# Performance work log

Measured on AMD Instinct MI355X. Metric: run time of the kernel, lower is better.

The kernel has to match this reference:

```python
import jax, jax.numpy as jnp
import numpy as np

# Module constants (from init_kwargs + mp_num=8 from the mesh)
D_MODEL = 1024
N_HEAD = 16
D_HEAD = 64
D_ROT = 64
MP = 8
B, S = 2, 2048
LOCAL = N_HEAD * D_HEAD // MP          # 128 : per-mp-shard qkv dim
F_IN = N_HEAD * D_HEAD * 3 + D_MODEL * 8  # 11264 : fused qkv+ff projection width
D_OUT_IN = D_MODEL + 4 * D_MODEL       # 5120 : attn (1024) + glu (4096) into output_proj
LN_EPS = 1e-5


def _rotate_every_two(x):
    # x: [..., d] with d even -> interleaved (-x2, x1)
    x1 = x[..., ::2]
    x2 = x[..., 1::2]
    return jnp.stack((-x2, x1), axis=-1).reshape(*x.shape[:-1], -1)


def _fixed_pos_embedding(seq_len, dim):
    inv_freq = 1.0 / (10000.0 ** (np.arange(0, dim, 2) / dim))
    t = np.einsum('i,j->ij', np.arange(seq_len), inv_freq)  # [S, dim//2]
    return jnp.asarray(np.sin(t), jnp.float32), jnp.asarray(np.cos(t), jnp.float32)


def _apply_rotary(x, sin, cos):
    # x: [B, S, mp, D_ROT]; sin/cos: [S, D_ROT//2]
    sin = jnp.repeat(sin, 2, axis=-1)[-x.shape[-3]:, None, :]  # [S,1,D_ROT]
    cos = jnp.repeat(cos, 2, axis=-1)[-x.shape[-3]:, None, :]
    return x * cos + _rotate_every_two(x) * sin


def setup_inputs() -> dict:
    key = jax.random.key(0)
    ks = jax.random.split(key, 4)
    x = jax.random.normal(ks[0], (B, S, D_MODEL), jnp.float32)
    attn_bias = jnp.zeros((1, S, S), jnp.float32)
    ln_scale = jnp.ones((D_MODEL,), jnp.float32)
    ln_offset = jnp.zeros((D_MODEL,), jnp.float32)
    w_in = jax.random.normal(ks[1], (D_MODEL, F_IN), jnp.float32) / np.sqrt(D_MODEL)
    b_in = jnp.zeros((F_IN,), jnp.float32)
    w_out = jax.random.normal(ks[2], (D_OUT_IN, D_MODEL), jnp.float32) / np.sqrt(D_MODEL)
    b_out = jnp.zeros((D_MODEL,), jnp.float32)
    return {"x": x, "attn_bias": attn_bias, "ln_scale": ln_scale, "ln_offset": ln_offset,
            "w_in": w_in, "b_in": b_in, "w_out": w_out, "b_out": b_out}


def reference(x, attn_bias, ln_scale, ln_offset, w_in, b_in, w_out, b_out):
    b, s, d = x.shape
    # LayerNorm (create_scale=True, create_offset=True, eps=1e-5)
    mu = jnp.mean(x, axis=-1, keepdims=True)
    var = jnp.var(x, axis=-1, keepdims=True)
    h = (x - mu) * jax.lax.rsqrt(var + LN_EPS) * ln_scale + ln_offset
    # fused QKV + FF projection, then mp split: [B,S,mp,F_IN/mp]
    proj = (h @ w_in + b_in).reshape(b, s, MP, -1)
    q, v, k, ff = jnp.split(proj, [LOCAL, 2 * LOCAL, 3 * LOCAL], axis=-1)
    # rotary on the first D_ROT dims of each mp shard (head_split is a shape no-op)
    sin, cos = _fixed_pos_embedding(s, D_ROT)
    q = jnp.concatenate([_apply_rotary(q[..., :D_ROT], sin, cos), q[..., D_ROT:]], axis=-1)
    k = jnp.concatenate([_apply_rotary(k[..., :D_ROT], sin, cos), k[..., D_ROT:]], axis=-1)
    # attention over h=mp shard-heads of dim LOCAL; scaled by sqrt(d_head) per source
    scale = np.sqrt(D_HEAD).astype(x.dtype)
    logits = jnp.einsum('bthd,bThd->bhtT', q, k) / scale  # [B,MP,S,S]
    causal = jnp.tril(jnp.ones((s, s), x.dtype))[None]
    bias = -1e10 * (1.0 - causal) + attn_bias
    weights = jax.nn.softmax(logits + bias, axis=-1)
    attn_vec = jnp.einsum('bhtT,bThd->bthd', weights, v)  # [B,S,MP,LOCAL]
    # GLU FFN (jax.nn.gelu default = tanh approximation, as in source)
    ff_out, ff_gate = jnp.split(ff, 2, axis=-1)
    glu = ff_out * jax.nn.gelu(ff_gate)  # [B,S,MP,4*D_MODEL/MP]
    # output: concat per-shard then flatten -> output_proj
    out = jnp.concatenate([attn_vec, glu], axis=-1).reshape(b, s, -1)  # [B,S,5120]
    return out @ w_out + b_out
```

## Files before the change

kernel.cpp:

```cpp
#include <hip/hip_runtime.h>
#include <stdint.h>

#define B_   2
#define S_   2048
#define DM   1024
#define FIN  11264
#define DOUT 5120
#define NSH  8
#define DH   128
#define ROWS (B_*S_)

typedef __attribute__((ext_vector_type(8))) __bf16 bf16x8;
typedef __attribute__((ext_vector_type(4))) __bf16 bf16x4;
typedef __attribute__((ext_vector_type(4))) float  f32x4;

union U2 { unsigned int u; __bf16 h[2]; };

__device__ __forceinline__ void gload16(const void* g, void* l) {
    __builtin_amdgcn_global_load_lds((const __attribute__((address_space(1))) void*)g,
                                     (__attribute__((address_space(3))) void*)l, 16, 0, 0);
}

__device__ __forceinline__ int origcol(int c) {
    if (c < 3072) { int p = c / 384; return p*1408 + (c - p*384); }
    int q = c - 3072; int p = q >> 10; int w = q & 1023;
    int a = w >> 5, g = (w >> 4) & 1, u = w & 15;
    return p*1408 + 384 + g*512 + a*16 + u;
}

__global__ __launch_bounds__(256) void ln_kernel(const float* __restrict__ x,
                                                 const float* __restrict__ sc,
                                                 const float* __restrict__ of,
                                                 __bf16* __restrict__ h) {
    int row = blockIdx.x, t = threadIdx.x;
    const float4 v = *(const float4*)&x[(size_t)row*DM + t*4];
    float s  = v.x + v.y + v.z + v.w;
    float ss = v.x*v.x + v.y*v.y + v.z*v.z + v.w*v.w;
#pragma unroll
    for (int off = 32; off >= 1; off >>= 1) {
        s  += __shfl_xor(s, off);
        ss += __shfl_xor(ss, off);
    }
    __shared__ float rs_[4], rss_[4];
    int wid = t >> 6, lane = t & 63;
    if (lane == 0) { rs_[wid] = s; rss_[wid] = ss; }
    __syncthreads();
    s  = rs_[0] + rs_[1] + rs_[2] + rs_[3];
    ss = rss_[0] + rss_[1] + rss_[2] + rss_[3];
    float mu  = s * (1.f/DM);
    float var = ss * (1.f/DM) - mu*mu;
    float r   = rsqrtf(var + 1e-5f);
    float4 scv = *(const float4*)&sc[t*4];
    float4 ofv = *(const float4*)&of[t*4];
    bf16x4 o;
    o[0] = (__bf16)((v.x-mu)*r*scv.x + ofv.x);
    o[1] = (__bf16)((v.y-mu)*r*scv.y + ofv.y);
    o[2] = (__bf16)((v.z-mu)*r*scv.z + ofv.z);
    o[3] = (__bf16)((v.w-mu)*r*scv.w + ofv.w);
    *(bf16x4*)&h[(size_t)row*DM + t*4] = o;
}

__global__ __launch_bounds__(256) void transpose_kernel(const float* __restrict__ in,
                                                        __bf16* __restrict__ out,
                                                        int R, int C) {
    __shared__ __bf16 tile[64][72];
    int c0 = blockIdx.x * 64, r0 = blockIdx.y * 64;
    int t = threadIdx.x;
#pragma unroll
    for (int it = 0; it < 4; ++it) {
        int flat = it*1024 + t*4;
        int rl = flat >> 6, cl = flat & 63;
        float4 v = *(const float4*)&in[(size_t)(r0+rl)*C + c0 + cl];
        tile[rl][cl+0] = (__bf16)v.x;
        tile[rl][cl+1] = (__bf16)v.y;
        tile[rl][cl+2] = (__bf16)v.z;
        tile[rl][cl+3] = (__bf16)v.w;
    }
    __syncthreads();
#pragma unroll
    for (int it = 0; it < 4; ++it) {
        int flat = it*1024 + t*4;
        int cl = flat >> 6, rl = flat & 63;
        bf16x4 o;
#pragma unroll
        for (int j = 0; j < 4; ++j) o[j] = tile[rl+j][cl];
        *(bf16x4*)&out[(size_t)(c0+cl)*R + r0 + rl] = o;
    }
}

__global__ __launch_bounds__(256) void transpose_perm_kernel(const float* __restrict__ in,
                                                             __bf16* __restrict__ out) {
    __shared__ __bf16 tile[64][72];
    int c0 = blockIdx.x * 64, r0 = blockIdx.y * 64;
    int t = threadIdx.x;
#pragma unroll
    for (int it = 0; it < 4; ++it) {
        int flat = it*1024 + t*4;
        int rl = flat >> 6, cl = flat & 63;
        int oc = origcol(c0 + cl);
        float4 v = *(const float4*)&in[(size_t)(r0+rl)*FIN + oc];
        tile[rl][cl+0] = (__bf16)v.x;
        tile[rl][cl+1] = (__bf16)v.y;
        tile[rl][cl+2] = (__bf16)v.z;
        tile[rl][cl+3] = (__bf16)v.w;
    }
    __syncthreads();
#pragma unroll
    for (int it = 0; it < 4; ++it) {
        int flat = it*1024 + t*4;
        int cl = flat >> 6, rl = flat & 63;
        bf16x4 o;
#pragma unroll
        for (int j = 0; j < 4; ++j) o[j] = tile[rl+j][cl];
        *(bf16x4*)&out[(size_t)(c0+cl)*DM + r0 + rl] = o;
    }
}

__global__ __launch_bounds__(256) void permbias_kernel(const float* __restrict__ b_in,
                                                       float* __restrict__ bp) {
    int c = blockIdx.x * 256 + threadIdx.x;
    if (c < FIN) bp[c] = b_in[origcol(c)];
}

#define MFMA4(ACCI, BN) \
    acc[ACCI][BN] = __builtin_amdgcn_mfma_f32_16x16x32_bf16(a[(ACCI)&3][0], b[BN][0], acc[ACCI][BN],0,0,0); \
    acc[ACCI][BN] = __builtin_amdgcn_mfma_f32_16x16x32_bf16(a[(ACCI)&3][1], b[BN][1], acc[ACCI][BN],0,0,0);

__global__ __launch_bounds__(512, 2) void gemm256_kernel(const __bf16* __restrict__ A,
                                                         const __bf16* __restrict__ BT,
                                                         const float* __restrict__ bias,
                                                         __bf16* __restrict__ Cqvk,
                                                         __bf16* __restrict__ Cglu,
                                                         float* __restrict__ Cf,
                                                         int M, int N, int K, int klen) {
    __shared__ __align__(16) char lds[131072];
    int t = threadIdx.x, wid = t >> 6, lane = t & 63;
    int wr = wid >> 2, wc = wid & 3;
    int fr = lane & 15, fq = lane >> 4;
    int kbeg = blockIdx.z * klen;
    int nbx = gridDim.x;
    int bid = blockIdx.y * nbx + blockIdx.x;
    int cpx = (nbx * gridDim.y) >> 3;
    int swz = (bid & 7) * cpx + (bid >> 3);
    int bx = swz % nbx, by = swz / nbx;
    int m0 = by * 256, n0 = bx * 256;

    const __bf16* srcA[4];
    const __bf16* srcB[4];
#pragma unroll
    for (int j = 0; j < 4; ++j) {
        int F = (j*512 + t) * 16;
        int lr = F >> 7, c = (F & 127) ^ ((lr & 7) << 4);
        srcA[j] = A + (size_t)(m0 + lr) * K + kbeg + (c >> 1);
        int row = ((lr >> 5) & 3) * 64 + (lr >> 7) * 32 + (lr & 31);
        srcB[j] = BT + (size_t)(n0 + row) * K + kbeg + (c >> 1);
    }
    int lrAlo[4], lrAhi[4], lrB[4];
#pragma unroll
    for (int i = 0; i < 4; ++i) {
        lrAlo[i] = (wr*128 + i*16 + fr) * 128;
        lrAhi[i] = lrAlo[i] + 64*128;
    }
#pragma unroll
    for (int n = 0; n < 4; ++n)
        lrB[n] = ((n >> 1)*128 + wc*32 + (n & 1)*16 + fr) * 128;
    int swzb = (fr & 7) << 4;
    int cb00 = (fq*16) ^ swzb;
    int cb01 = (64 + fq*16) ^ swzb;

    f32x4 acc[8][4] = {};
    gload16(srcA[0], lds +     0 + wid*1024);
    gload16(srcA[2], lds + 16384 + wid*1024);
    gload16(srcB[0], lds + 32768 + wid*1024);
    gload16(srcB[1], lds + 40960 + wid*1024);
    gload16(srcB[2], lds + 49152 + wid*1024);
    gload16(srcB[3], lds + 57344 + wid*1024);
    gload16(srcA[1], lds +  8192 + wid*1024);
    gload16(srcA[3], lds + 24576 + wid*1024);
    asm volatile("s_waitcnt vmcnt(4)" ::: "memory");
    __builtin_amdgcn_s_barrier();

    int nit = klen >> 6;
    for (int it = 0; it < nit; ++it) {
        const char* bc = lds + (it & 1) * 65536;
        char* bn = lds + ((it & 1) ^ 1) * 65536;
        const char* bcB = bc + 32768;
        int koff = (it + 1) << 6;
        bool pf = (it + 1 < nit);
        bf16x8 a[4][2], b[4][2];
#pragma unroll
        for (int i = 0; i < 4; ++i) {
            a[i][0] = *(const bf16x8*)(bc + lrAlo[i] + cb00);
            a[i][1] = *(const bf16x8*)(bc + lrAlo[i] + cb01);
        }
        b[0][0] = *(const bf16x8*)(bcB + lrB[0] + cb00);
        b[0][1] = *(const bf16x8*)(bcB + lrB[0] + cb01);
        b[1][0] = *(const bf16x8*)(bcB + lrB[1] + cb00);
        b[1][1] = *(const bf16x8*)(bcB + lrB[1] + cb01);
        if (pf) {
            gload16(srcA[0] + koff, bn +     0 + wid*1024);
            gload16(srcA[2] + koff, bn + 16384 + wid*1024);
            gload16(srcB[0] + koff, bn + 32768 + wid*1024);
            gload16(srcB[1] + koff, bn + 40960 + wid*1024);
            gload16(srcB[2] + koff, bn + 49152 + wid*1024);
            gload16(srcB[3] + koff, bn + 57344 + wid*1024);
            gload16(srcA[1] + koff, bn +  8192 + wid*1024);
            gload16(srcA[3] + koff, bn + 24576 + wid*1024);
        }
        __builtin_amdgcn_s_setprio(1);
#pragma unroll
        for (int i = 0; i < 4; ++i) { MFMA4(i,0) MFMA4(i,1) }
        __builtin_amdgcn_s_setprio(0);
        if (pf) asm volatile("s_waitcnt vmcnt(10)" ::: "memory");
        else    asm volatile("s_waitcnt vmcnt(2)" ::: "memory");
        __builtin_amdgcn_s_barrier();
        b[2][0] = *(const bf16x8*)(bcB + lrB[2] + cb00);
        b[2][1] = *(const bf16x8*)(bcB + lrB[2] + cb01);
        b[3][0] = *(const bf16x8*)(bcB + lrB[3] + cb00);
        b[3][1] = *(const bf16x8*)(bcB + lrB[3] + cb01);
        __builtin_amdgcn_s_setprio(1);
#pragma unroll
        for (int i = 0; i < 4; ++i) { MFMA4(i,2) MFMA4(i,3) }
        __builtin_amdgcn_s_setprio(0);
        if (pf) asm volatile("s_waitcnt vmcnt(8)" ::: "memory");
        else    asm volatile("s_waitcnt vmcnt(0)" ::: "memory");
        __builtin_amdgcn_s_barrier();
#pragma unroll
        for (int i = 0; i < 4; ++i) {
            a[i][0] = *(const bf16x8*)(bc + lrAhi[i] + cb00);
            a[i][1] = *(const bf16x8*)(bc + lrAhi[i] + cb01);
        }
        __builtin_amdgcn_s_setprio(1);
#pragma unroll
        for (int i = 0; i < 4; ++i) { MFMA4(4+i,0) MFMA4(4+i,1) MFMA4(4+i,2) MFMA4(4+i,3) }
        __builtin_amdgcn_s_setprio(0);
        if (pf) {
            asm volatile("s_waitcnt vmcnt(4)" ::: "memory");
            __builtin_amdgcn_s_barrier();
        }
    }
    if (Cf) {
        float* Cz = Cf + (size_t)blockIdx.z * M * N;
#pragma unroll
        for (int i = 0; i < 8; ++i)
#pragma unroll
            for (int n = 0; n < 4; ++n) {
                int col = n0 + wc*64 + (n >> 1)*32 + (n & 1)*16 + fr;
#pragma unroll
                for (int r = 0; r < 4; ++r) {
                    int row = m0 + wr*128 + i*16 + fq*4 + r;
                    Cz[(size_t)row*N + col] = acc[i][n][r];
                }
            }
    } else if (n0 < 3072) {
#pragma unroll
        for (int i = 0; i < 8; ++i)
#pragma unroll
            for (int n = 0; n < 4; ++n) {
                int col = n0 + wc*64 + (n >> 1)*32 + (n & 1)*16 + fr;
                float bv = bias[col];
#pragma unroll
                for (int r = 0; r < 4; ++r) {
                    int row = m0 + wr*128 + i*16 + fq*4 + r;
                    Cqvk[(size_t)row*3072 + col] = (__bf16)(acc[i][n][r] + bv);
                }
            }
    } else {
        int q = n0 - 3072;
        int p = q >> 10;
#pragma unroll
        for (int m = 0; m < 2; ++m) {
            int off = wc*64 + m*32;
            float bo = bias[n0 + off + fr];
            float bg = bias[n0 + off + 16 + fr];
            int j = (((q & 1023) + off) >> 5) * 16 + fr;
            int colg = p*640 + 128 + j;
#pragma unroll
            for (int i = 0; i < 8; ++i)
#pragma unroll
                for (int r = 0; r < 4; ++r) {
                    int row = m0 + wr*128 + i*16 + fq*4 + r;
                    float ov = acc[i][2*m][r] + bo;
                    float gv = acc[i][2*m+1][r] + bg;
                    float e2 = __expf(1.5957691216057308f*(gv + 0.044715f*gv*gv*gv));
                    float gl = gv * (1.f - 1.f/(e2 + 1.f));
                    Cglu[(size_t)row*DOUT + colg] = (__bf16)(ov * gl);
                }
        }
    }
}

__global__ __launch_bounds__(256) void addbias_kernel(const float* __restrict__ pk,
                                                      const float* __restrict__ bias,
                                                      float* __restrict__ out) {
    int idx = blockIdx.x * 256 + threadIdx.x;
    const size_t stride = (size_t)ROWS * DM / 4;
    float4 a0 = ((const float4*)pk)[idx];
    float4 a1 = ((const float4*)pk)[idx + stride];
    float4 a2 = ((const float4*)pk)[idx + 2*stride];
    float4 a3 = ((const float4*)pk)[idx + 3*stride];
    float4 bb = ((const float4*)bias)[idx & 255];
    float4 o;
    o.x = a0.x + a1.x + a2.x + a3.x + bb.x;
    o.y = a0.y + a1.y + a2.y + a3.y + bb.y;
    o.z = a0.z + a1.z + a2.z + a3.z + bb.z;
    o.w = a0.w + a1.w + a2.w + a3.w + bb.w;
    ((float4*)out)[idx] = o;
}

__global__ __launch_bounds__(256) void rqkv_kernel(const __bf16* __restrict__ proj2,
                                                   __bf16* __restrict__ qh,
                                                   __bf16* __restrict__ kh,
                                                   __bf16* __restrict__ vt) {
    __shared__ __bf16 tile[64*144];
    int r0 = blockIdx.x * 64;
    int p  = blockIdx.y;
    int t  = threadIdx.x;
    int b  = r0 >> 11;
    int bh = b*NSH + p;
#pragma unroll
    for (int j = 0; j < 4; ++j) {
        int e = (j*256 + t) * 8;
        int sl = e >> 7, d = e & 127;
        const __bf16* rowp = proj2 + (size_t)(r0 + sl)*3072 + p*384;
        bf16x8 vq = *(const bf16x8*)&rowp[d];
        bf16x8 vv = *(const bf16x8*)&rowp[128 + d];
        bf16x8 vk = *(const bf16x8*)&rowp[256 + d];
        int s = (r0 + sl) & (S_ - 1);
        if (d < 64) {
#pragma unroll
            for (int u = 0; u < 4; ++u) {
                int i = (d >> 1) + u;
                float inv = exp2f(-(float)i * 0.4152410118609203f);
                float ang = (float)s * inv;
                float cn = __cosf(ang), sn = __sinf(ang);
                float q0 = vq[2*u], q1 = vq[2*u+1];
                float k0 = vk[2*u], k1 = vk[2*u+1];
                vq[2*u]   = (__bf16)(q0*cn - q1*sn);
                vq[2*u+1] = (__bf16)(q1*cn + q0*sn);
                vk[2*u]   = (__bf16)(k0*cn - k1*sn);
                vk[2*u+1] = (__bf16)(k1*cn + k0*sn);
            }
        }
#pragma unroll
        for (int u = 0; u < 8; ++u) vq[u] = (__bf16)((float)vq[u] * 0.125f);
        size_t o = ((size_t)bh * S_ + s) * DH + d;
        *(bf16x8*)&qh[o] = vq;
        *(bf16x8*)&kh[o] = vk;
        int ch = ((d >> 3) + sl) & 15;
        *(bf16x8*)&tile[sl*144 + ch*8] = vv;
    }
    __syncthreads();
#pragma unroll
    for (int j = 0; j < 4; ++j) {
        int e = (j*256 + t) * 8;
        int d = e >> 6, sb = e & 63;
        bf16x8 o;
#pragma unroll
        for (int u = 0; u < 8; ++u) {
            int sl = sb + u;
            int ch = ((d >> 3) + sl) & 15;
            o[u] = tile[sl*144 + ch*8 + (d & 7)];
        }
        size_t ov = ((size_t)bh * DH + d) * S_ + (r0 & (S_ - 1)) + sb;
        *(bf16x8*)&vt[ov] = o;
    }
}

__device__ __forceinline__ void stage_kv(const __bf16* Kb, const __bf16* Vg,
                                         char* KsB, char* VsB,
                                         int kvbase, int t, int wid) {
#pragma unroll
    for (int j = 0; j < 4; ++j) {
        int F = (j*256 + t)*16;
        int r = F >> 8, c = F & 255;
        gload16(Kb + (size_t)(kvbase + r)*DH + ((c ^ ((r & 7) << 4)) >> 1),
                KsB + j*4096 + (wid << 10));
    }
#pragma unroll
    for (int j = 0; j < 4; ++j) {
        int F = (j*256 + t)*16;
        int r = F >> 7, c = F & 127;
        gload16(Vg + (size_t)r*S_ + kvbase + ((c ^ ((r & 7) << 4)) >> 1),
                VsB + j*4096 + (wid << 10));
    }
}

__global__ __launch_bounds__(256, 2) void attn_kernel(const __bf16* __restrict__ qh,
                                                      const __bf16* __restrict__ kh,
                                                      const __bf16* __restrict__ vt,
                                                      const float* __restrict__ ab,
                                                      __bf16* __restrict__ ag) {
    __shared__ __bf16 Ks[2*8192];
    __shared__ __bf16 Vs[2*8192];
    __shared__ __bf16 Ps[4][16*72];
    int bh = blockIdx.y;
    int b = bh >> 3, hh = bh & 7;
    int xr = blockIdx.x;
    int qb = (xr & 1) ? (31 - (xr >> 1)) : (xr >> 1);
    int q0 = qb * 64;
    int t = threadIdx.x, wid = t >> 6, lane = t & 63;
    int fr = lane & 15, fkb = (lane >> 4) * 16;
    const __bf16* Qb = qh + (size_t)bh * S_ * DH;
    const __bf16* Kb = kh + (size_t)bh * S_ * DH;
    const __bf16* Vg = vt + (size_t)bh * DH * S_;
    bf16x8 qf[4];
#pragma unroll
    for (int kk = 0; kk < 4; ++kk)
        qf[kk] = *(const bf16x8*)&Qb[(size_t)(q0 + wid*16 + fr)*DH + kk*32 + (lane>>4)*8];
    float m[4] = {-3e38f, -3e38f, -3e38f, -3e38f};
    float l[4] = {0.f, 0.f, 0.f, 0.f};
    f32x4 o[8] = {};
    int rowb = q0 + wid*16 + (lane >> 4)*4;
    int nit = qb + 1;
    stage_kv(Kb, Vg, (char*)Ks, (char*)Vs, 0, t, wid);
    for (int it = 0; it < nit; ++it) {
        int kv0 = it * 64, cur = it & 1;
        float abv[4][4];
#pragma unroll
        for (int n = 0; n < 4; ++n)
#pragma unroll
            for (int r = 0; r < 4; ++r)
                abv[n][r] = ab[(size_t)(rowb + r)*S_ + kv0 + n*16 + fr];
        if (it + 1 < nit) {
            stage_kv(Kb, Vg, (char*)Ks + (cur^1)*16384, (char*)Vs + (cur^1)*16384,
                     kv0 + 64, t, wid);
            asm volatile("s_waitcnt vmcnt(8)" ::: "memory");
        } else {
            asm volatile("s_waitcnt vmcnt(0)" ::: "memory");
        }
        __builtin_amdgcn_s_barrier();
        const char* KsC = (const char*)Ks + cur*16384;
        float pv[4][4];
        __builtin_amdgcn_s_setprio(1);
#pragma unroll
        for (int n = 0; n < 4; ++n) {
            f32x4 sacc = {};
#pragma unroll
            for (int kk = 0; kk < 4; ++kk) {
                int row = n*16 + fr;
                int c2 = (kk*64 + fkb) ^ ((fr & 7) << 4);
                bf16x8 kf = *(const bf16x8*)(KsC + row*256 + c2);
                sacc = __builtin_amdgcn_mfma_f32_16x16x32_bf16(qf[kk], kf, sacc, 0, 0, 0);
            }
#pragma unroll
            for (int r = 0; r < 4; ++r) pv[n][r] = sacc[r];
        }
        __builtin_amdgcn_s_setprio(0);
#pragma unroll
        for (int n = 0; n < 4; ++n) {
            int col = kv0 + n*16 + fr;
#pragma unroll
            for (int r = 0; r < 4; ++r)
                pv[n][r] += abv[n][r] + (col <= rowb + r ? 0.f : -1e10f);
        }
        float alpha[4];
#pragma unroll
        for (int r = 0; r < 4; ++r) {
            float mx = fmaxf(fmaxf(pv[0][r], pv[1][r]), fmaxf(pv[2][r], pv[3][r]));
#pragma unroll
            for (int off = 8; off >= 1; off >>= 1) mx = fmaxf(mx, __shfl_xor(mx, off));
            float mn = fmaxf(m[r], mx);
            alpha[r] = __expf(m[r] - mn);
            m[r] = mn;
            float sum = 0.f;
#pragma unroll
            for (int n = 0; n < 4; ++n) { pv[n][r] = __expf(pv[n][r] - mn); sum += pv[n][r]; }
#pragma unroll
            for (int off = 8; off >= 1; off >>= 1) sum += __shfl_xor(sum, off);
            l[r] = l[r]*alpha[r] + sum;
        }
#pragma unroll
        for (int nf = 0; nf < 8; ++nf)
#pragma unroll
            for (int r = 0; r < 4; ++r) o[nf][r] *= alpha[r];
#pragma unroll
        for (int n = 0; n < 4; ++n)
#pragma unroll
            for (int r = 0; r < 4; ++r)
                Ps[wid][((lane >> 4)*4 + r)*72 + n*16 + fr] = (__bf16)pv[n][r];
        asm volatile("s_waitcnt lgkmcnt(0)" ::: "memory");
        __builtin_amdgcn_sched_barrier(0);
        bf16x8 pf[2];
#pragma unroll
        for (int kk = 0; kk < 2; ++kk)
            pf[kk] = *(const bf16x8*)&Ps[wid][fr*72 + kk*32 + (lane>>4)*8];
        const char* VsC = (const char*)Vs + cur*16384;
        __builtin_amdgcn_s_setprio(1);
#pragma unroll
        for (int nf = 0; nf < 8; ++nf) {
#pragma unroll
            for (int kk = 0; kk < 2; ++kk) {
                int row = nf*16 + fr;
                int c2 = (kk*64 + fkb) ^ ((fr & 7) << 4);
                bf16x8 vf = *(const bf16x8*)(VsC + row*128 + c2);
                o[nf] = __builtin_amdgcn_mfma_f32_16x16x32_bf16(pf[kk], vf, o[nf], 0, 0, 0);
            }
        }
        __builtin_amdgcn_s_setprio(0);
        asm volatile("s_waitcnt lgkmcnt(0)" ::: "memory");
        __builtin_amdgcn_sched_barrier(0);
        __builtin_amdgcn_s_barrier();
    }
    int rq = (lane >> 4) * 4;
#pragma unroll
    for (int r = 0; r < 4; ++r) {
        float inv = 1.f / l[r];
#pragma unroll
        for (int nf = 0; nf < 8; ++nf) {
            int qr = q0 + wid*16 + rq + r;
            int d = nf*16 + fr;
            ag[((size_t)(b*S_ + qr))*DOUT + hh*640 + d] = (__bf16)(o[nf][r] * inv);
        }
    }
}

extern "C" void kernel_launch(void* const* d_in, const int* in_sizes, int n_in,
                              void* d_out, int out_size, void* d_ws, size_t ws_size,
                              hipStream_t stream) {
    const float* x     = (const float*)d_in[0];
    const float* ab    = (const float*)d_in[1];
    const float* lns   = (const float*)d_in[2];
    const float* lno   = (const float*)d_in[3];
    const float* w_in  = (const float*)d_in[4];
    const float* b_in  = (const float*)d_in[5];
    const float* w_out = (const float*)d_in[6];
    const float* b_out = (const float*)d_in[7];
    float* out = (float*)d_out;
    char* ws = (char*)d_ws;

    __bf16* w_in_t  = (__bf16*)(ws);
    __bf16* w_out_t = (__bf16*)(ws +  23068672);
    __bf16* hbuf    = (__bf16*)(ws +  33554432);
    __bf16* proj2   = (__bf16*)(ws +  41943040);
    __bf16* vtb     = (__bf16*)(ws +  67108864);
    __bf16* qh      = (__bf16*)(ws +  75497472);
    __bf16* kh      = (__bf16*)(ws +  83886080);
    __bf16* agb     = (__bf16*)(ws +  92274688);
    float*  pk      = (float*)(ws + 134217728);
    float*  bperm   = (float*)(ws + 134217728);

    transpose_perm_kernel<<<dim3(FIN/64, DM/64), 256, 0, stream>>>(w_in, w_in_t);
    transpose_kernel<<<dim3(DM/64, DOUT/64), 256, 0, stream>>>(w_out, w_out_t, DOUT, DM);
    permbias_kernel<<<(FIN + 255)/256, 256, 0, stream>>>(b_in, bperm);
    ln_kernel<<<ROWS, 256, 0, stream>>>(x, lns, lno, hbuf);
    gemm256_kernel<<<dim3(FIN/256, ROWS/256, 1), 512, 0, stream>>>(hbuf, w_in_t, bperm,
                                                                   proj2, agb, nullptr,
                                                                   ROWS, FIN, DM, DM);
    rqkv_kernel<<<dim3(ROWS/64, NSH), 256, 0, stream>>>(proj2, qh, kh, vtb);
    attn_kernel<<<dim3(S_/64, B_*NSH), 256, 0, stream>>>(qh, kh, vtb, ab, agb);
    gemm256_kernel<<<dim3(DM/256, ROWS/256, 4), 512, 0, stream>>>(agb, w_out_t, nullptr,
                                                                  nullptr, nullptr, pk,
                                                                  ROWS, DM, DOUT, DOUT/4);
    addbias_kernel<<<ROWS*DM/1024, 256, 0, stream>>>(pk, b_out, out);
}
```

Before: 292.6 us.

## Use dedicated 128x128 split-K=2 GEMM for output projection

The output projection moves off the 256x256 split-K=4 GEMM onto a new simpler 128x128 tile kernel with 256 threads, split-K of 2 and a single LDS buffer synchronised per K step. The grid goes from 4x16x4 to 8x32x2 blocks, and the bias reduction now reads two partials instead of four, which cuts partial-sum traffic. The first GEMM is specialised with compile-time shapes. The new kernel has no double buffering or prefetch overlap, so per-block efficiency may fall even as occupancy and the reduction cost improve.

```diff
diff --git a/kernel.cpp b/kernel.cpp
--- a/kernel.cpp
+++ b/kernel.cpp
@@ -126,18 +126,16 @@
     acc[ACCI][BN] = __builtin_amdgcn_mfma_f32_16x16x32_bf16(a[(ACCI)&3][0], b[BN][0], acc[ACCI][BN],0,0,0); \
     acc[ACCI][BN] = __builtin_amdgcn_mfma_f32_16x16x32_bf16(a[(ACCI)&3][1], b[BN][1], acc[ACCI][BN],0,0,0);
 
-__global__ __launch_bounds__(512, 2) void gemm256_kernel(const __bf16* __restrict__ A,
-                                                         const __bf16* __restrict__ BT,
-                                                         const float* __restrict__ bias,
-                                                         __bf16* __restrict__ Cqvk,
-                                                         __bf16* __restrict__ Cglu,
-                                                         float* __restrict__ Cf,
-                                                         int M, int N, int K, int klen) {
+__global__ __launch_bounds__(512, 2) void gemm1_kernel(const __bf16* __restrict__ A,
+                                                       const __bf16* __restrict__ BT,
+                                                       const float* __restrict__ bias,
+                                                       __bf16* __restrict__ Cqvk,
+                                                       __bf16* __restrict__ Cglu) {
+    const int M = ROWS, N = FIN, K = DM;
     __shared__ __align__(16) char lds[131072];
     int t = threadIdx.x, wid = t >> 6, lane = t & 63;
     int wr = wid >> 2, wc = wid & 3;
     int fr = lane & 15, fq = lane >> 4;
-    int kbeg = blockIdx.z * klen;
     int nbx = gridDim.x;
     int bid = blockIdx.y * nbx + blockIdx.x;
     int cpx = (nbx * gridDim.y) >> 3;
@@ -151,9 +149,9 @@
     for (int j = 0; j < 4; ++j) {
         int F = (j*512 + t) * 16;
         int lr = F >> 7, c = (F & 127) ^ ((lr & 7) << 4);
-        srcA[j] = A + (size_t)(m0 + lr) * K + kbeg + (c >> 1);
+        srcA[j] = A + (size_t)(m0 + lr) * K + (c >> 1);
         int row = ((lr >> 5) & 3) * 64 + (lr >> 7) * 32 + (lr & 31);
-        srcB[j] = BT + (size_t)(n0 + row) * K + kbeg + (c >> 1);
+        srcB[j] = BT + (size_t)(n0 + row) * K + (c >> 1);
     }
     int lrAlo[4], lrAhi[4], lrB[4];
 #pragma unroll
@@ -180,7 +178,7 @@
     asm volatile("s_waitcnt vmcnt(4)" ::: "memory");
     __builtin_amdgcn_s_barrier();
 
-    int nit = klen >> 6;
+    int nit = K >> 6;
     for (int it = 0; it < nit; ++it) {
         const char* bc = lds + (it & 1) * 65536;
         char* bn = lds + ((it & 1) ^ 1) * 65536;
@@ -239,20 +237,7 @@
             __builtin_amdgcn_s_barrier();
         }
     }
-    if (Cf) {
-        float* Cz = Cf + (size_t)blockIdx.z * M * N;
-#pragma unroll
-        for (int i = 0; i < 8; ++i)
-#pragma unroll
-            for (int n = 0; n < 4; ++n) {
-                int col = n0 + wc*64 + (n >> 1)*32 + (n & 1)*16 + fr;
-#pragma unroll
-                for (int r = 0; r < 4; ++r) {
-                    int row = m0 + wr*128 + i*16 + fq*4 + r;
-                    Cz[(size_t)row*N + col] = acc[i][n][r];
-                }
-            }
-    } else if (n0 < 3072) {
+    if (n0 < 3072) {
 #pragma unroll
         for (int i = 0; i < 8; ++i)
 #pragma unroll
@@ -290,21 +275,100 @@
     }
 }
 
-__global__ __launch_bounds__(256) void addbias_kernel(const float* __restrict__ pk,
-                                                      const float* __restrict__ bias,
-                                                      float* __restrict__ out) {
+__global__ __launch_bounds__(256, 4) void gemm2_kernel(const __bf16* __restrict__ A,
+                                                       const __bf16* __restrict__ BT,
+                                                       float* __restrict__ P,
+                                                       int klen) {
+    const int M = ROWS, N = DM, K = DOUT;
+    __shared__ __align__(16) char lds[32768];
+    int t = threadIdx.x, wid = t >> 6, lane = t & 63;
+    int wm = (wid >> 1) * 64, wn = (wid & 1) * 64;
+    int fr = lane & 15, fq = lane >> 4;
+    int kbeg = blockIdx.z * klen;
+    int nbx = gridDim.x;
+    int bid = blockIdx.y * nbx + blockIdx.x;
+    int cpx = (nbx * gridDim.y) >> 3;
+    int swz = (bid & 7) * cpx + (bid >> 3);
+    int bx = swz % nbx, by = swz / nbx;
+    int m0 = by * 128, n0 = bx * 128;
+
+    const __bf16* srcA[4];
+    const __bf16* srcB[4];
+#pragma unroll
+    for (int j = 0; j < 4; ++j) {
+        int F = (j*256 + t) * 16;
+        int row = F >> 7;
+        int c = (F & 127) ^ ((row & 7) << 4);
+        srcA[j] = A  + (size_t)(m0 + row) * K + kbeg + (c >> 1);
+        srcB[j] = BT + (size_t)(n0 + row) * K + kbeg + (c >> 1);
+    }
+    int rowA[4], rowB[4];
+#pragma unroll
+    for (int i = 0; i < 4; ++i) {
+        rowA[i] = (wm + i*16 + fr) * 128;
+        rowB[i] = 16384 + (wn + i*16 + fr) * 128;
+    }
+    int swzb = (fr & 7) << 4;
+    int cb0 = (fq*16) ^ swzb;
+    int cb1 = (64 + fq*16) ^ swzb;
+
+    f32x4 acc[4][4] = {};
+    for (int k0 = 0; k0 < klen; k0 += 64) {
+#pragma unroll
+        for (int j = 0; j < 4; ++j)
+            gload16(srcA[j] + k0, lds + j*4096 + wid*1024);
+#pragma unroll
+        for (int j = 0; j < 4; ++j)
+            gload16(srcB[j] + k0, lds + 16384 + j*4096 + wid*1024);
+        __syncthreads();
+        bf16x8 a[4], b[4];
+#pragma unroll
+        for (int i = 0; i < 4; ++i) a[i] = *(const bf16x8*)(lds + rowA[i] + cb0);
+#pragma unroll
+        for (int n = 0; n < 4; ++n) b[n] = *(const bf16x8*)(lds + rowB[n] + cb0);
+#pragma unroll
+        for (int i = 0; i < 4; ++i)
+#pragma unroll
+            for (int n = 0; n < 4; ++n)
+                acc[i][n] = __builtin_amdgcn_mfma_f32_16x16x32_bf16(a[i], b[n], acc[i][n], 0, 0, 0);
+#pragma unroll
+        for (int i = 0; i < 4; ++i) a[i] = *(const bf16x8*)(lds + rowA[i] + cb1);
+#pragma unroll
+        for (int n = 0; n < 4; ++n) b[n] = *(const bf16x8*)(lds + rowB[n] + cb1);
+#pragma unroll
+        for (int i = 0; i < 4; ++i)
+#pragma unroll
+            for (int n = 0; n < 4; ++n)
+                acc[i][n] = __builtin_amdgcn_mfma_f32_16x16x32_bf16(a[i], b[n], acc[i][n], 0, 0, 0);
+        __syncthreads();
+    }
+    float* Pz = P + (size_t)blockIdx.z * M * N;
+#pragma unroll
+    for (int i = 0; i < 4; ++i)
+#pragma unroll
+        for (int n = 0; n < 4; ++n) {
+            int col = n0 + wn + n*16 + fr;
+#pragma unroll
+            for (int r = 0; r < 4; ++r) {
+                int row = m0 + wm + i*16 + fq*4 + r;
+                Pz[(size_t)row*N + col] = acc[i][n][r];
+            }
+        }
+}
+
+__global__ __launch_bounds__(256) void addbias2_kernel(const float* __restrict__ pk,
+                                                       const float* __restrict__ bias,
+                                                       float* __restrict__ out) {
     int idx = blockIdx.x * 256 + threadIdx.x;
     const size_t stride = (size_t)ROWS * DM / 4;
     float4 a0 = ((const float4*)pk)[idx];
     float4 a1 = ((const float4*)pk)[idx + stride];
-    float4 a2 = ((const float4*)pk)[idx + 2*stride];
-    float4 a3 = ((const float4*)pk)[idx + 3*stride];
     float4 bb = ((const float4*)bias)[idx & 255];
     float4 o;
-    o.x = a0.x + a1.x + a2.x + a3.x + bb.x;
-    o.y = a0.y + a1.y + a2.y + a3.y + bb.y;
-    o.z = a0.z + a1.z + a2.z + a3.z + bb.z;
-    o.w = a0.w + a1.w + a2.w + a3.w + bb.w;
+    o.x = a0.x + a1.x + bb.x;
+    o.y = a0.y + a1.y + bb.y;
+    o.z = a0.z + a1.z + bb.z;
+    o.w = a0.w + a1.w + bb.w;
     ((float4*)out)[idx] = o;
 }
 
@@ -538,19 +602,16 @@
     __bf16* kh      = (__bf16*)(ws +  83886080);
     __bf16* agb     = (__bf16*)(ws +  92274688);
     float*  pk      = (float*)(ws + 134217728);
-    float*  bperm   = (float*)(ws + 134217728);
+    float*  bperm   = (float*)(ws + 167772160);
 
     transpose_perm_kernel<<<dim3(FIN/64, DM/64), 256, 0, stream>>>(w_in, w_in_t);
     transpose_kernel<<<dim3(DM/64, DOUT/64), 256, 0, stream>>>(w_out, w_out_t, DOUT, DM);
     permbias_kernel<<<(FIN + 255)/256, 256, 0, stream>>>(b_in, bperm);
     ln_kernel<<<ROWS, 256, 0, stream>>>(x, lns, lno, hbuf);
-    gemm256_kernel<<<dim3(FIN/256, ROWS/256, 1), 512, 0, stream>>>(hbuf, w_in_t, bperm,
-                                                                   proj2, agb, nullptr,
-                                                                   ROWS, FIN, DM, DM);
+    gemm1_kernel<<<dim3(FIN/256, ROWS/256), 512, 0, stream>>>(hbuf, w_in_t, bperm,
+                                                              proj2, agb);
     rqkv_kernel<<<dim3(ROWS/64, NSH), 256, 0, stream>>>(proj2, qh, kh, vtb);
     attn_kernel<<<dim3(S_/64, B_*NSH), 256, 0, stream>>>(qh, kh, vtb, ab, agb);
-    gemm256_kernel<<<dim3(DM/256, ROWS/256, 4), 512, 0, stream>>>(agb, w_out_t, nullptr,
-                                                                  nullptr, nullptr, pk,
-                                                                  ROWS, DM, DOUT, DOUT/4);
-    addbias_kernel<<<ROWS*DM/1024, 256, 0, stream>>>(pk, b_out, out);
-}
+    gemm2_kernel<<<dim3(DM/128, ROWS/128, 2), 256, 0, stream>>>(agb, w_out_t, pk, DOUT/2);
+    addbias2_kernel<<<ROWS*DM/1024, 256, 0, stream>>>(pk, b_out, out);
+}
```

After: 287.2 us. No clear change (-1.9%).
